# Optimization experiments

Hardware: AMD Instinct MI355X
Metric: run time of the kernel (lower is better)

Reference implementation:

```python
import jax, jax.numpy as jnp
import numpy as np

B, T, IMG = 64, 20, 64
IN_DIM = IMG * IMG          # 4096, from x.view(B,-1,64*64)
C_IN = 8                    # input_channels
R_DIM = C_IN * 1024         # 8192, reshape(B,20,-1,32,32) constraint
NF = 64                     # num_filters
Z_DIM = 256
LIN_IN = 2 * NF * 7 * 7     # 6272


def setup_inputs() -> dict:
    key = jax.random.key(0)
    ks = jax.random.split(key, 10)
    x = jax.random.normal(ks[0], (B, T, IMG, IMG), jnp.float32)
    Win = jax.random.normal(ks[1], (IN_DIM, R_DIM), jnp.float32) / np.sqrt(IN_DIM).astype(np.float32)
    U = jax.random.normal(ks[2], (IN_DIM, R_DIM), jnp.float32) / np.sqrt(IN_DIM).astype(np.float32)
    Wr = jax.random.normal(ks[3], (R_DIM, R_DIM), jnp.float32) / np.sqrt(R_DIM).astype(np.float32)
    conv1_w = jax.random.normal(ks[4], (NF, C_IN, 3, 3, 3), jnp.float32) * 0.05
    conv1_b = jax.random.normal(ks[5], (NF,), jnp.float32) * 0.01
    conv2_w = jax.random.normal(ks[6], (2 * NF, NF, 3, 4, 4), jnp.float32) * 0.05
    conv2_b = jax.random.normal(ks[7], (2 * NF,), jnp.float32) * 0.01
    lin_w = jax.random.normal(ks[8], (Z_DIM, LIN_IN), jnp.float32) * 0.02
    lin_b = jax.random.normal(ks[9], (Z_DIM,), jnp.float32) * 0.01
    return {"x": x, "Win": Win, "U": U, "Wr": Wr,
            "conv1_w": conv1_w, "conv1_b": conv1_b,
            "conv2_w": conv2_w, "conv2_b": conv2_b,
            "lin_w": lin_w, "lin_b": lin_b}


def reference(x, Win, U, Wr, conv1_w, conv1_b, conv2_w, conv2_b, lin_w, lin_b):
    Bn = x.shape[0]
    xf = x.reshape(Bn, T, IN_DIM)                      # (B,T,4096)
    h0 = jnp.tanh(xf[:, 0] @ Win)                      # (B,R)
    xU = jnp.einsum('bti,ir->tbr', xf[:, 1:], U)       # precompute input drive (T-1,B,R)

    def step(h, xu):
        h = jnp.tanh(xu + h @ Wr)
        return h, h

    _, hs = jax.lax.scan(step, h0, xU)                 # (T-1,B,R)
    H = jnp.concatenate([h0[None], hs], axis=0)        # (T,B,R)
    H = jnp.swapaxes(H, 0, 1)                          # (B,T,R)

    h = H.reshape(Bn, T, C_IN, 32, 32).transpose(0, 2, 1, 3, 4)  # (B,C,T,32,32)
    dn = ('NCDHW', 'OIDHW', 'NCDHW')
    y = jax.lax.conv_general_dilated(h, conv1_w, (1, 2, 2),
                                     [(1, 1), (1, 1), (1, 1)], dimension_numbers=dn)
    y = y + conv1_b[None, :, None, None, None]
    y = jax.nn.leaky_relu(y, 0.01)                     # (B,NF,20,16,16)
    y = jax.lax.conv_general_dilated(y, conv2_w, (1, 2, 2),
                                     [(1, 1), (0, 0), (0, 0)], dimension_numbers=dn)
    y = y + conv2_b[None, :, None, None, None]
    y = jax.nn.leaky_relu(y, 0.01)                     # (B,2NF,20,7,7)

    y = y.reshape(Bn, -1, T, LIN_IN)                   # (B,1,20,6272), same row-major view as torch
    y = y @ lin_w.T + lin_b                            # (B,1,20,Z_DIM)
    mu, log_var = jnp.split(y, 2, axis=3)
    return mu, log_var
```

## Files before the change

### kernel.cpp

```cpp
#include <hip/hip_runtime.h>

typedef __bf16 v8bf __attribute__((ext_vector_type(8)));
typedef float  v4f  __attribute__((ext_vector_type(4)));
typedef unsigned short us8 __attribute__((ext_vector_type(8)));

__device__ __forceinline__ float bf2f(unsigned short u) {
    union { unsigned int i; float f; } v; v.i = ((unsigned int)u) << 16; return v.f;
}
__device__ __forceinline__ unsigned short f2bf(float f) {
    union { float f; unsigned int i; } v; v.f = f;
    return (unsigned short)((v.i + 0x7fffu + ((v.i >> 16) & 1u)) >> 16);
}
__device__ __forceinline__ int sw(int b) { return b ^ (((b >> 7) & 7) << 4); }

__global__ __launch_bounds__(256)
void transpose_f32_bf16(const float* __restrict__ src,
                        unsigned short* __restrict__ dst, int K, int N)
{
    __shared__ unsigned short tile[64][72];
    const int tid = threadIdx.x;
    const int c0 = blockIdx.x * 64, r0 = blockIdx.y * 64;
    const int tr = tid >> 2, tc4 = tid & 3;
    const float* sp = src + (size_t)(r0 + tr) * N + c0 + tc4 * 16;
#pragma unroll
    for (int j = 0; j < 4; ++j) {
        v4f f = *reinterpret_cast<const v4f*>(sp + j * 4);
#pragma unroll
        for (int e = 0; e < 4; ++e) tile[tr][tc4 * 16 + j * 4 + e] = f2bf(f[e]);
    }
    __syncthreads();
    const int ow = tid >> 3, och = tid & 7;
#pragma unroll
    for (int p = 0; p < 2; ++p) {
        int orow = p * 32 + ow;
        us8 o;
#pragma unroll
        for (int e = 0; e < 8; ++e) o[e] = tile[och * 8 + e][orow];
        *reinterpret_cast<us8*>(dst + (size_t)(c0 + orow) * K + r0 + och * 8) = o;
    }
}

template<int BN, bool STORE_BF16, bool AF32, bool BF32>
__global__ __launch_bounds__(256, 2)
void gemm_bt(const void* __restrict__ Ap, int lda_lo, int lda_hi,
             const void* __restrict__ BTp, int ldb,
             void* __restrict__ Cout, int ldc,
             int ksub, long long csplit_stride)
{
    constexpr int FN  = BN / 32;
    constexpr int BCH = BN / 32;
    const int tid = threadIdx.x;
    const int lane = tid & 63, wid = tid >> 6;
    const int wr = wid >> 1, wc = wid & 1;
    const int nt = blockIdx.x, mt = blockIdx.y, kz = blockIdx.z;
    const int n0 = nt * BN;
    const int kstart = kz * ksub;

    __shared__ unsigned short smem[(64 + BN) * 64];
    char* As = reinterpret_cast<char*>(smem);
    char* Bs = reinterpret_cast<char*>(smem + 64 * 64);

    const unsigned short* A16 = (const unsigned short*)Ap;
    const float*          A32 = (const float*)Ap;
    const unsigned short* B16 = (const unsigned short*)BTp;
    const float*          B32 = (const float*)BTp;

    const int arow = AF32 ? (tid >> 2) : (tid >> 3);
    const int aq   = AF32 ? (tid & 3) : (tid & 7);
    const float* Ab32 = A32 + (size_t)arow * lda_lo + (size_t)mt * lda_hi + kstart + aq * 16;
    const unsigned short* Ab16 = A16 + (size_t)arow * lda_lo + (size_t)mt * lda_hi + kstart + aq * 8;
    const int brow = tid >> 3, bq = tid & 7;
    const float* Bb32 = B32 + (size_t)(n0 + brow) * ldb + kstart + bq * 8;
    const unsigned short* Bb16 = B16 + (size_t)(n0 + brow) * ldb + kstart + bq * 8;

    v4f fa[4];
    us8 ra[2];
    v4f fb[BCH][2];
    us8 rb[BCH];

    auto load = [&](int kk) {
        if (AF32) {
#pragma unroll
            for (int j = 0; j < 4; ++j)
                fa[j] = *reinterpret_cast<const v4f*>(Ab32 + kk + j * 4);
        } else {
#pragma unroll
            for (int p = 0; p < 2; ++p)
                ra[p] = *reinterpret_cast<const us8*>(Ab16 + (size_t)(p * 32) * lda_lo + kk);
        }
        if (BF32) {
#pragma unroll
            for (int p = 0; p < BCH; ++p) {
                fb[p][0] = *reinterpret_cast<const v4f*>(Bb32 + (size_t)(p * 32) * ldb + kk);
                fb[p][1] = *reinterpret_cast<const v4f*>(Bb32 + (size_t)(p * 32) * ldb + kk + 4);
            }
        } else {
#pragma unroll
            for (int p = 0; p < BCH; ++p)
                rb[p] = *reinterpret_cast<const us8*>(Bb16 + (size_t)(p * 32) * ldb + kk);
        }
    };
    auto stage = [&]() {
        if (AF32) {
#pragma unroll
            for (int h = 0; h < 2; ++h) {
                us8 v;
#pragma unroll
                for (int e = 0; e < 8; ++e) v[e] = f2bf(fa[h * 2 + (e >> 2)][e & 3]);
                *reinterpret_cast<us8*>(As + arow * 128 + (((aq * 2 + h) * 16) ^ ((arow & 7) << 4))) = v;
            }
        } else {
#pragma unroll
            for (int p = 0; p < 2; ++p)
                *reinterpret_cast<us8*>(As + (arow + p * 32) * 128 + ((aq * 16) ^ ((arow & 7) << 4))) = ra[p];
        }
#pragma unroll
        for (int p = 0; p < BCH; ++p) {
            us8 v;
            if (BF32) {
#pragma unroll
                for (int e = 0; e < 8; ++e) v[e] = f2bf(fb[p][e >> 2][e & 3]);
            } else v = rb[p];
            *reinterpret_cast<us8*>(Bs + (brow + p * 32) * 128 + ((bq * 16) ^ ((brow & 7) << 4))) = v;
        }
    };

    v4f z4 = {0.f, 0.f, 0.f, 0.f};
    v4f acc[2][FN];
#pragma unroll
    for (int i = 0; i < 2; ++i)
#pragma unroll
        for (int j = 0; j < FN; ++j) acc[i][j] = z4;

    const int l15 = lane & 15, l4 = lane >> 4;
    const int nk = ksub / 64;
    load(0);
    for (int it = 0; it < nk; ++it) {
        __syncthreads();
        stage();
        __syncthreads();
        if (it + 1 < nk) load((it + 1) * 64);
#pragma unroll
        for (int ks = 0; ks < 2; ++ks) {
            const int kb = (ks * 32 + l4 * 8) * 2;
            v8bf af[2], bfr[FN];
#pragma unroll
            for (int fm = 0; fm < 2; ++fm) {
                int row = wr * 32 + fm * 16 + l15;
                af[fm] = *reinterpret_cast<const v8bf*>(As + row * 128 + (kb ^ ((row & 7) << 4)));
            }
#pragma unroll
            for (int fn = 0; fn < FN; ++fn) {
                int row = wc * (BN / 2) + fn * 16 + l15;
                bfr[fn] = *reinterpret_cast<const v8bf*>(Bs + row * 128 + (kb ^ ((row & 7) << 4)));
            }
#pragma unroll
            for (int fm = 0; fm < 2; ++fm)
#pragma unroll
                for (int fn = 0; fn < FN; ++fn)
                    acc[fm][fn] = __builtin_amdgcn_mfma_f32_16x16x32_bf16(af[fm], bfr[fn], acc[fm][fn], 0, 0, 0);
        }
    }
    const long long m0 = (long long)mt * 64;
#pragma unroll
    for (int fm = 0; fm < 2; ++fm)
#pragma unroll
        for (int fn = 0; fn < FN; ++fn)
#pragma unroll
            for (int r = 0; r < 4; ++r) {
                long long row = m0 + wr * 32 + fm * 16 + l4 * 4 + r;
                long long col = n0 + wc * (BN / 2) + fn * 16 + l15;
                long long idx = (long long)kz * csplit_stride + row * ldc + col;
                if (STORE_BF16) reinterpret_cast<unsigned short*>(Cout)[idx] = f2bf(acc[fm][fn][r]);
                else            reinterpret_cast<float*>(Cout)[idx]          = acc[fm][fn][r];
            }
}

__global__ __launch_bounds__(256)
void scan_combine(const float* __restrict__ part, int nparts,
                  const unsigned short* __restrict__ xu,
                  unsigned short* __restrict__ hcur,
                  unsigned short* __restrict__ Hbf, int t)
{
    int i = blockIdx.x * 256 + threadIdx.x;
    float pre = xu ? bf2f(xu[i]) : 0.f;
    for (int z = 0; z < nparts; ++z) pre += part[(size_t)z * 524288 + i];
    float h = tanhf(pre);
    unsigned short hb = f2bf(h);
    hcur[i] = hb;
    int b = i >> 13, r = i & 8191;
    int c = r >> 10, pp = r & 1023;
    Hbf[(((size_t)b * 20 + t) * 1024 + pp) * 8 + c] = hb;
}

#define KZ 4
__global__ __launch_bounds__(256, 2)
void scan_step(const unsigned short* __restrict__ WrT,
               const unsigned short* __restrict__ hprev,
               const unsigned short* __restrict__ xu,
               unsigned short* __restrict__ hnext,
               unsigned short* __restrict__ Hbf, int t,
               float* __restrict__ part,
               unsigned int* __restrict__ tickets)
{
    const int tid = threadIdx.x, lane = tid & 63, wid = tid >> 6;
    const int wr = wid >> 1, wc = wid & 1;
    const int nt = blockIdx.x & 127, kz = blockIdx.x >> 7;
    const int n0 = nt * 64, kstart = kz * 2048;
    const int l15 = lane & 15, l4 = lane >> 4;

    __shared__ unsigned short smem[16384];
    char* base = reinterpret_cast<char*>(smem);

    const int srow = tid >> 3, sq = tid & 7;
    const int gslot = sq ^ (srow & 7);
    const unsigned short* Asrc = hprev + (size_t)srow * 8192 + kstart + gslot * 8;
    const unsigned short* Bsrc = WrT + (size_t)(n0 + srow) * 8192 + kstart + gslot * 8;

    auto stage = [&](int buf, int kk) {
        char* dA = base + buf * 16384 + wid * 1024;
        char* dB = dA + 8192;
#pragma unroll
        for (int p = 0; p < 2; ++p) {
            __builtin_amdgcn_global_load_lds(
                (const __attribute__((address_space(1))) void*)(Asrc + kk + (size_t)p * 32 * 8192),
                (__attribute__((address_space(3))) void*)(dA + p * 4096), 16, 0, 0);
            __builtin_amdgcn_global_load_lds(
                (const __attribute__((address_space(1))) void*)(Bsrc + kk + (size_t)p * 32 * 8192),
                (__attribute__((address_space(3))) void*)(dB + p * 4096), 16, 0, 0);
        }
    };

    v4f acc00 = {0.f, 0.f, 0.f, 0.f};
    v4f acc01 = acc00, acc10 = acc00, acc11 = acc00;

    stage(0, 0);
    for (int it = 0; it < 32; ++it) {
        const int cur = it & 1;
        __syncthreads();
        if (it + 1 < 32) stage(cur ^ 1, (it + 1) * 64);
        const char* As = base + cur * 16384;
        const char* Bs = As + 8192;
#pragma unroll
        for (int ks = 0; ks < 2; ++ks) {
            const int kb = (ks * 32 + l4 * 8) * 2;
            v8bf a0, a1, b0, b1;
            { int row = wr * 32 + l15;      a0 = *reinterpret_cast<const v8bf*>(As + row * 128 + (kb ^ ((row & 7) << 4))); }
            { int row = wr * 32 + 16 + l15; a1 = *reinterpret_cast<const v8bf*>(As + row * 128 + (kb ^ ((row & 7) << 4))); }
            { int row = wc * 32 + l15;      b0 = *reinterpret_cast<const v8bf*>(Bs + row * 128 + (kb ^ ((row & 7) << 4))); }
            { int row = wc * 32 + 16 + l15; b1 = *reinterpret_cast<const v8bf*>(Bs + row * 128 + (kb ^ ((row & 7) << 4))); }
            acc00 = __builtin_amdgcn_mfma_f32_16x16x32_bf16(a0, b0, acc00, 0, 0, 0);
            acc01 = __builtin_amdgcn_mfma_f32_16x16x32_bf16(a0, b1, acc01, 0, 0, 0);
            acc10 = __builtin_amdgcn_mfma_f32_16x16x32_bf16(a1, b0, acc10, 0, 0, 0);
            acc11 = __builtin_amdgcn_mfma_f32_16x16x32_bf16(a1, b1, acc11, 0, 0, 0);
        }
    }

    float* mypart = part + (size_t)kz * 524288;
#pragma unroll
    for (int r = 0; r < 4; ++r) {
        int row0 = wr * 32 + l4 * 4 + r;
        int col0 = n0 + wc * 32 + l15;
        mypart[(size_t)row0 * 8192 + col0]             = acc00[r];
        mypart[(size_t)row0 * 8192 + col0 + 16]        = acc01[r];
        mypart[(size_t)(row0 + 16) * 8192 + col0]      = acc10[r];
        mypart[(size_t)(row0 + 16) * 8192 + col0 + 16] = acc11[r];
    }

    __shared__ int lastflag;
    __syncthreads();
    if (tid == 0) {
        unsigned int old = __hip_atomic_fetch_add(&tickets[nt], 1u,
                              __ATOMIC_ACQ_REL, __HIP_MEMORY_SCOPE_AGENT);
        lastflag = (old == KZ - 1);
    }
    __syncthreads();
    if (!lastflag) return;

    const int row = tid >> 2;
    const int c0 = n0 + (tid & 3) * 16;
    float pre[16];
    {
        const us8* xp = reinterpret_cast<const us8*>(xu + (size_t)row * 8192 + c0);
        us8 x0 = xp[0], x1 = xp[1];
#pragma unroll
        for (int j = 0; j < 8; ++j) { pre[j] = bf2f(x0[j]); pre[8 + j] = bf2f(x1[j]); }
    }
#pragma unroll
    for (int z = 0; z < KZ; ++z) {
        const float* pp = part + (size_t)z * 524288 + (size_t)row * 8192 + c0;
#pragma unroll
        for (int q = 0; q < 4; ++q) {
            v4f v = *reinterpret_cast<const v4f*>(pp + q * 4);
#pragma unroll
            for (int e = 0; e < 4; ++e) pre[q * 4 + e] += v[e];
        }
    }
    us8 o0, o1;
#pragma unroll
    for (int j = 0; j < 16; ++j) {
        unsigned short hb = f2bf(tanhf(pre[j]));
        if (j < 8) o0[j] = hb; else o1[j - 8] = hb;
        int col = c0 + j;
        Hbf[(((size_t)row * 20 + t) * 1024 + (col & 1023)) * 8 + (col >> 10)] = hb;
    }
    *reinterpret_cast<us8*>(hnext + (size_t)row * 8192 + c0)     = o0;
    *reinterpret_cast<us8*>(hnext + (size_t)row * 8192 + c0 + 8) = o1;
    if (tid == 0)
        __hip_atomic_store(&tickets[nt], 0u, __ATOMIC_RELAXED, __HIP_MEMORY_SCOPE_AGENT);
}

__global__ __launch_bounds__(256)
void cvt_w1(const float* __restrict__ w, unsigned short* __restrict__ o,
            unsigned int* __restrict__ tickets)
{
    if (blockIdx.x == 0 && threadIdx.x < 128) tickets[threadIdx.x] = 0;
    int idx = blockIdx.x * 256 + threadIdx.x;
    if (idx >= 64 * 224) return;
    int co = idx / 224, k = idx % 224;
    int g = k >> 3, ci = k & 7;
    float v = 0.f;
    if (g < 27) {
        int dt = g / 9, rr = g % 9, dy = rr / 3, dx = rr % 3;
        v = w[(((co * 8 + ci) * 3 + dt) * 3 + dy) * 3 + dx];
    }
    o[idx] = f2bf(v);
}
__global__ __launch_bounds__(256)
void cvt_w2(const float* __restrict__ w, unsigned short* __restrict__ o)
{
    int idx = blockIdx.x * 256 + threadIdx.x;
    if (idx >= 128 * 3072) return;
    int co = idx / 3072, k = idx % 3072;
    int g = k >> 6, ci = k & 63;
    int dt = g >> 4, dy = (g >> 2) & 3, dx = g & 3;
    o[idx] = f2bf(w[(((co * 64 + ci) * 3 + dt) * 4 + dy) * 4 + dx]);
}

__global__ __launch_bounds__(256, 2)
void conv1_kernel(const unsigned short* __restrict__ H,
                  const unsigned short* __restrict__ w1,
                  const float* __restrict__ bias,
                  unsigned short* __restrict__ y1)
{
    const int b = blockIdx.x, t = blockIdx.y;
    const int tid = threadIdx.x, lane = tid & 63, wid = tid >> 6;
    __shared__ unsigned short in_s[3 * 33 * 33 * 8];
    __shared__ unsigned short w_s[64 * 224];

    for (int i = tid; i < 13068; i += 256) reinterpret_cast<unsigned int*>(in_s)[i] = 0;
    __syncthreads();
    for (int idx = tid; idx < 3 * 1024; idx += 256) {
        int dt = idx >> 10, rem = idx & 1023;
        int iy = rem >> 5, ix = rem & 31;
        int ts = t + dt - 1;
        if (ts >= 0 && ts < 20) {
            us8 v = *reinterpret_cast<const us8*>(H + (((size_t)b * 20 + ts) * 1024 + rem) * 8);
            int byte = ((dt * 33 + iy + 1) * 33 + (ix + 1)) * 16;
            *reinterpret_cast<us8*>(reinterpret_cast<char*>(in_s) + sw(byte)) = v;
        }
    }
    for (int idx = tid; idx < 64 * 28; idx += 256) {
        int co = idx / 28, j = idx % 28;
        us8 v = *reinterpret_cast<const us8*>(w1 + co * 224 + j * 8);
        *reinterpret_cast<us8*>(reinterpret_cast<char*>(w_s) + sw(co * 448 + j * 16)) = v;
    }
    __syncthreads();

    const int l15 = lane & 15, l4 = lane >> 4;
    const int m_lo = wid * 64 + l15;
    v4f z4 = {0.f, 0.f, 0.f, 0.f};
    v4f acc[4][4];
#pragma unroll
    for (int i = 0; i < 4; ++i)
#pragma unroll
        for (int j = 0; j < 4; ++j) acc[i][j] = z4;

#pragma unroll
    for (int ks = 0; ks < 7; ++ks) {
        int g = ks * 4 + l4;
        int gc = g < 27 ? g : 26;
        int dt = gc / 9, rr = gc % 9, dy = rr / 3, dx = rr % 3;
        v8bf ap[4], aw[4];
#pragma unroll
        for (int fm = 0; fm < 4; ++fm) {
            int m = fm * 16 + m_lo;
            int py = m >> 4, px = m & 15;
            int byte = ((dt * 33 + 2 * py + dy) * 33 + 2 * px + dx) * 16;
            ap[fm] = *reinterpret_cast<const v8bf*>(reinterpret_cast<const char*>(in_s) + sw(byte));
        }
        int kb2 = (ks * 32 + l4 * 8) * 2;
#pragma unroll
        for (int fc = 0; fc < 4; ++fc) {
            int co = fc * 16 + l15;
            aw[fc] = *reinterpret_cast<const v8bf*>(reinterpret_cast<const char*>(w_s) + sw(co * 448 + kb2));
        }
#pragma unroll
        for (int fm = 0; fm < 4; ++fm)
#pragma unroll
            for (int fc = 0; fc < 4; ++fc)
                acc[fm][fc] = __builtin_amdgcn_mfma_f32_16x16x32_bf16(ap[fm], aw[fc], acc[fm][fc], 0, 0, 0);
    }
#pragma unroll
    for (int fm = 0; fm < 4; ++fm)
#pragma unroll
        for (int fc = 0; fc < 4; ++fc)
#pragma unroll
            for (int r = 0; r < 4; ++r) {
                int m  = wid * 64 + fm * 16 + l4 * 4 + r;
                int co = fc * 16 + l15;
                float v = acc[fm][fc][r] + bias[co];
                v = v > 0.f ? v : 0.01f * v;
                y1[(((size_t)b * 20 + t) * 256 + m) * 64 + co] = f2bf(v);
            }
}

__global__ __launch_bounds__(512, 2)
void conv2_kernel(const unsigned short* __restrict__ y1,
                  const unsigned short* __restrict__ w2,
                  const float* __restrict__ bias,
                  unsigned short* __restrict__ y2)
{
    const int b = blockIdx.x, t = blockIdx.y;
    const int tid = threadIdx.x, lane = tid & 63, wid = tid >> 6;
    const int wc = wid >> 1, wr = wid & 1;
    __shared__ unsigned short in_s[256 * 64];
    __shared__ unsigned short w_s[128 * 128];
    const int l15 = lane & 15, l4 = lane >> 4;

    const int m0v = wr * 32 + l15, m1v = m0v + 16;
    const int m0c = m0v < 49 ? m0v : 48, m1c = m1v < 49 ? m1v : 48;
    const int py0 = m0c / 7, px0 = m0c - py0 * 7;
    const int py1 = m1c / 7, px1 = m1c - py1 * 7;

    v4f acc[2][2];
#pragma unroll
    for (int i = 0; i < 2; ++i)
#pragma unroll
        for (int j = 0; j < 2; ++j) acc[i][j] = (v4f){0.f, 0.f, 0.f, 0.f};

    for (int dt = 0; dt < 3; ++dt) {
        int ts = t + dt - 1;
        __syncthreads();
        if (ts < 0 || ts >= 20) continue;
#pragma unroll
        for (int p = 0; p < 4; ++p) {
            int idx = tid + p * 512;
            int slot = idx >> 3, c8 = idx & 7;
            int yy = slot >> 4, xx = slot & 15;
            us8 v = *reinterpret_cast<const us8*>(y1 + (((size_t)b * 20 + ts) * 256 + slot) * 64 + c8 * 8);
            int cell = ((yy & 1) * 2 + (xx & 1)) * 64 + (yy >> 1) * 8 + (xx >> 1);
            int byte = cell * 128 + ((c8 * 16) ^ (((cell ^ (cell >> 3)) & 7) << 4));
            *reinterpret_cast<us8*>(reinterpret_cast<char*>(in_s) + byte) = v;
        }
        for (int kc = 0; kc < 8; ++kc) {
            __syncthreads();
#pragma unroll
            for (int p = 0; p < 4; ++p) {
                int idx = tid + p * 512;
                int co = idx >> 4, j = idx & 15;
                us8 v = *reinterpret_cast<const us8*>(w2 + (size_t)co * 3072 + dt * 1024 + kc * 128 + j * 8);
                *reinterpret_cast<us8*>(reinterpret_cast<char*>(w_s) + co * 256 + ((j * 16) ^ ((co & 7) << 4))) = v;
            }
            __syncthreads();
#pragma unroll
            for (int ks = 0; ks < 4; ++ks) {
                int klocal = ks * 32 + l4 * 8;
                int kk = kc * 128 + klocal;
                int dy = (kk >> 8) & 3, dx = (kk >> 6) & 3, ci0 = kk & 63;
                v8bf aw[2], bp[2];
#pragma unroll
                for (int fc = 0; fc < 2; ++fc) {
                    int co = wc * 32 + fc * 16 + l15;
                    aw[fc] = *reinterpret_cast<const v8bf*>(reinterpret_cast<const char*>(w_s)
                               + co * 256 + ((klocal * 2) ^ ((co & 7) << 4)));
                }
                int plane = ((dy & 1) << 1) | (dx & 1);
                int c0 = plane * 64 + (py0 + (dy >> 1)) * 8 + px0 + (dx >> 1);
                int c1 = plane * 64 + (py1 + (dy >> 1)) * 8 + px1 + (dx >> 1);
                bp[0] = *reinterpret_cast<const v8bf*>(reinterpret_cast<const char*>(in_s)
                          + c0 * 128 + ((ci0 * 2) ^ (((c0 ^ (c0 >> 3)) & 7) << 4)));
                bp[1] = *reinterpret_cast<const v8bf*>(reinterpret_cast<const char*>(in_s)
                          + c1 * 128 + ((ci0 * 2) ^ (((c1 ^ (c1 >> 3)) & 7) << 4)));
#pragma unroll
                for (int fc = 0; fc < 2; ++fc)
#pragma unroll
                    for (int fm = 0; fm < 2; ++fm)
                        acc[fc][fm] = __builtin_amdgcn_mfma_f32_16x16x32_bf16(aw[fc], bp[fm], acc[fc][fm], 0, 0, 0);
            }
        }
    }
#pragma unroll
    for (int fc = 0; fc < 2; ++fc)
#pragma unroll
        for (int fm = 0; fm < 2; ++fm)
#pragma unroll
            for (int r = 0; r < 4; ++r) {
                int co = wc * 32 + fc * 16 + l4 * 4 + r;
                int m  = wr * 32 + fm * 16 + l15;
                if (m < 49) {
                    float v = acc[fc][fm][r] + bias[co];
                    v = v > 0.f ? v : 0.01f * v;
                    y2[(((size_t)b * 128 + co) * 20 + t) * 49 + m] = f2bf(v);
                }
            }
}

__global__ __launch_bounds__(256)
void lin_epi(const float* __restrict__ linC, const float* __restrict__ lb,
             float* __restrict__ out)
{
    int i = blockIdx.x * 256 + threadIdx.x;
    int m = i >> 8, n = i & 255;
    float v = lb[n];
#pragma unroll
    for (int z = 0; z < 7; ++z) v += linC[(size_t)z * 327680 + i];
    size_t o = (n < 128) ? ((size_t)m * 128 + n) : (163840 + (size_t)m * 128 + (n - 128));
    out[o] = v;
}

extern "C" void kernel_launch(void* const* d_in, const int* in_sizes, int n_in,
                              void* d_out, int out_size, void* d_ws, size_t ws_size,
                              hipStream_t stream)
{
    const float* x   = (const float*)d_in[0];
    const float* Win = (const float*)d_in[1];
    const float* U   = (const float*)d_in[2];
    const float* Wr  = (const float*)d_in[3];
    const float* c1w = (const float*)d_in[4];
    const float* c1b = (const float*)d_in[5];
    const float* c2w = (const float*)d_in[6];
    const float* c2b = (const float*)d_in[7];
    const float* lw  = (const float*)d_in[8];
    const float* lb  = (const float*)d_in[9];

    char* ws = (char*)d_ws;
    unsigned short* WrT  = (unsigned short*)(ws);
    unsigned short* WT   = (unsigned short*)(ws + 134217728ll);
    unsigned short* y1   = (unsigned short*)(ws + 134217728ll);
    unsigned short* y2   = (unsigned short*)(ws + 176160768ll);
    unsigned short* XALL = (unsigned short*)(ws + 201326592ll);
    unsigned short* Hbf  = (unsigned short*)(ws + 222298112ll);
    unsigned short* hb0  = (unsigned short*)(ws + 243269632ll);
    unsigned short* hb1  = (unsigned short*)(ws + 244318208ll);
    float*          part = (float*)        (ws + 245366784ll);
    float*          linC = (float*)        (ws + 245366784ll);
    unsigned short* w1bf = (unsigned short*)(ws + 254541824ll);
    unsigned short* w2bf = (unsigned short*)(ws + 254570496ll);
    unsigned int*   tick = (unsigned int*) (ws + 255356928ll);
    float*          out  = (float*)d_out;

    cvt_w1<<<56, 256, 0, stream>>>(c1w, w1bf, tick);
    cvt_w2<<<1536, 256, 0, stream>>>(c2w, w2bf);

    transpose_f32_bf16<<<dim3(128, 64), 256, 0, stream>>>(Win, WT, 4096, 8192);
    gemm_bt<64, false, true, false><<<dim3(128, 1, 4), 256, 0, stream>>>(
        x, 81920, 0, WT, 4096, part, 8192, 1024, 524288ll);
    scan_combine<<<2048, 256, 0, stream>>>(part, 4, (const unsigned short*)nullptr, hb0, Hbf, 0);

    transpose_f32_bf16<<<dim3(128, 64), 256, 0, stream>>>(U, WT, 4096, 8192);
    gemm_bt<128, true, true, false><<<dim3(64, 19, 1), 256, 0, stream>>>(
        x + 4096, 81920, 4096, WT, 4096, XALL + 524288, 8192, 4096, 0ll);

    transpose_f32_bf16<<<dim3(128, 128), 256, 0, stream>>>(Wr, WrT, 8192, 8192);
    for (int t = 1; t < 20; ++t) {
        const unsigned short* hprev = (t & 1) ? hb0 : hb1;
        unsigned short*       hnext = (t & 1) ? hb1 : hb0;
        scan_step<<<512, 256, 0, stream>>>(WrT, hprev, XALL + (size_t)t * 524288,
                                           hnext, Hbf, t, part, tick);
    }

    conv1_kernel<<<dim3(64, 20), 256, 0, stream>>>(Hbf, w1bf, c1b, y1);
    conv2_kernel<<<dim3(64, 20), 512, 0, stream>>>(y1, w2bf, c2b, y2);

    gemm_bt<128, false, false, true><<<dim3(2, 20, 7), 256, 0, stream>>>(
        y2, 6272, 6272 * 64, lw, 6272, linC, 256, 896, 327680ll);
    lin_epi<<<1280, 256, 0, stream>>>(linC, lb, out);
}
```

Baseline: 1.455 ms.

## Deepen scan_step prefetch to 4 stages and reuse it for the h0 GEMM

```diff
diff --git a/kernel.cpp b/kernel.cpp
--- a/kernel.cpp
+++ b/kernel.cpp
@@ -38,6 +38,19 @@
         for (int e = 0; e < 8; ++e) o[e] = tile[och * 8 + e][orow];
         *reinterpret_cast<us8*>(dst + (size_t)(c0 + orow) * K + r0 + och * 8) = o;
     }
+}
+
+__global__ __launch_bounds__(256)
+void cvt_x(const float* __restrict__ x, unsigned short* __restrict__ xb)
+{
+    int i = blockIdx.x * 256 + threadIdx.x;
+    if (i >= 655360) return;
+    v4f f0 = *reinterpret_cast<const v4f*>(x + (size_t)i * 8);
+    v4f f1 = *reinterpret_cast<const v4f*>(x + (size_t)i * 8 + 4);
+    us8 o;
+#pragma unroll
+    for (int e = 0; e < 4; ++e) { o[e] = f2bf(f0[e]); o[4 + e] = f2bf(f1[e]); }
+    *reinterpret_cast<us8*>(xb + (size_t)i * 8) = o;
 }
 
 template<int BN, bool STORE_BF16, bool AF32, bool BF32>
@@ -176,27 +189,11 @@
             }
 }
 
-__global__ __launch_bounds__(256)
-void scan_combine(const float* __restrict__ part, int nparts,
-                  const unsigned short* __restrict__ xu,
-                  unsigned short* __restrict__ hcur,
-                  unsigned short* __restrict__ Hbf, int t)
-{
-    int i = blockIdx.x * 256 + threadIdx.x;
-    float pre = xu ? bf2f(xu[i]) : 0.f;
-    for (int z = 0; z < nparts; ++z) pre += part[(size_t)z * 524288 + i];
-    float h = tanhf(pre);
-    unsigned short hb = f2bf(h);
-    hcur[i] = hb;
-    int b = i >> 13, r = i & 8191;
-    int c = r >> 10, pp = r & 1023;
-    Hbf[(((size_t)b * 20 + t) * 1024 + pp) * 8 + c] = hb;
-}
-
 #define KZ 4
 __global__ __launch_bounds__(256, 2)
-void scan_step(const unsigned short* __restrict__ WrT,
-               const unsigned short* __restrict__ hprev,
+void scan_step(const unsigned short* __restrict__ A, int lda,
+               const unsigned short* __restrict__ BT, int ldb,
+               int kper,
                const unsigned short* __restrict__ xu,
                unsigned short* __restrict__ hnext,
                unsigned short* __restrict__ Hbf, int t,
@@ -206,16 +203,17 @@
     const int tid = threadIdx.x, lane = tid & 63, wid = tid >> 6;
     const int wr = wid >> 1, wc = wid & 1;
     const int nt = blockIdx.x & 127, kz = blockIdx.x >> 7;
-    const int n0 = nt * 64, kstart = kz * 2048;
+    const int n0 = nt * 64, kstart = kz * kper;
     const int l15 = lane & 15, l4 = lane >> 4;
-
-    __shared__ unsigned short smem[16384];
+    const int nit = kper >> 6;
+
+    __shared__ unsigned short smem[32768];
     char* base = reinterpret_cast<char*>(smem);
 
     const int srow = tid >> 3, sq = tid & 7;
     const int gslot = sq ^ (srow & 7);
-    const unsigned short* Asrc = hprev + (size_t)srow * 8192 + kstart + gslot * 8;
-    const unsigned short* Bsrc = WrT + (size_t)(n0 + srow) * 8192 + kstart + gslot * 8;
+    const unsigned short* Asrc = A + (size_t)srow * lda + kstart + gslot * 8;
+    const unsigned short* Bsrc = BT + (size_t)(n0 + srow) * ldb + kstart + gslot * 8;
 
     auto stage = [&](int buf, int kk) {
         char* dA = base + buf * 16384 + wid * 1024;
@@ -223,10 +221,10 @@
 #pragma unroll
         for (int p = 0; p < 2; ++p) {
             __builtin_amdgcn_global_load_lds(
-                (const __attribute__((address_space(1))) void*)(Asrc + kk + (size_t)p * 32 * 8192),
+                (const __attribute__((address_space(1))) void*)(Asrc + kk + (size_t)p * 32 * lda),
                 (__attribute__((address_space(3))) void*)(dA + p * 4096), 16, 0, 0);
             __builtin_amdgcn_global_load_lds(
-                (const __attribute__((address_space(1))) void*)(Bsrc + kk + (size_t)p * 32 * 8192),
+                (const __attribute__((address_space(1))) void*)(Bsrc + kk + (size_t)p * 32 * ldb),
                 (__attribute__((address_space(3))) void*)(dB + p * 4096), 16, 0, 0);
         }
     };
@@ -234,12 +232,16 @@
     v4f acc00 = {0.f, 0.f, 0.f, 0.f};
     v4f acc01 = acc00, acc10 = acc00, acc11 = acc00;
 
-    stage(0, 0);
-    for (int it = 0; it < 32; ++it) {
-        const int cur = it & 1;
-        __syncthreads();
-        if (it + 1 < 32) stage(cur ^ 1, (it + 1) * 64);
-        const char* As = base + cur * 16384;
+    stage(0, 0); stage(1, 64); stage(2, 128);
+    for (int it = 0; it < nit; ++it) {
+        const int ahead = nit - 1 - it;
+        if (ahead >= 2)      asm volatile("s_waitcnt vmcnt(8)" ::: "memory");
+        else if (ahead == 1) asm volatile("s_waitcnt vmcnt(4)" ::: "memory");
+        else                 asm volatile("s_waitcnt vmcnt(0)" ::: "memory");
+        __builtin_amdgcn_s_barrier();
+        __builtin_amdgcn_sched_barrier(0);
+        if (it + 3 < nit) stage((it + 3) & 3, (it + 3) * 64);
+        const char* As = base + (it & 3) * 16384;
         const char* Bs = As + 8192;
 #pragma unroll
         for (int ks = 0; ks < 2; ++ks) {
@@ -280,11 +282,14 @@
     const int row = tid >> 2;
     const int c0 = n0 + (tid & 3) * 16;
     float pre[16];
-    {
+    if (xu) {
         const us8* xp = reinterpret_cast<const us8*>(xu + (size_t)row * 8192 + c0);
         us8 x0 = xp[0], x1 = xp[1];
 #pragma unroll
         for (int j = 0; j < 8; ++j) { pre[j] = bf2f(x0[j]); pre[8 + j] = bf2f(x1[j]); }
+    } else {
+#pragma unroll
+        for (int j = 0; j < 16; ++j) pre[j] = 0.f;
     }
 #pragma unroll
     for (int z = 0; z < KZ; ++z) {
@@ -536,6 +541,7 @@
 
     char* ws = (char*)d_ws;
     unsigned short* WrT  = (unsigned short*)(ws);
+    unsigned short* xbf  = (unsigned short*)(ws);
     unsigned short* WT   = (unsigned short*)(ws + 134217728ll);
     unsigned short* y1   = (unsigned short*)(ws + 134217728ll);
     unsigned short* y2   = (unsigned short*)(ws + 176160768ll);
@@ -552,11 +558,11 @@
 
     cvt_w1<<<56, 256, 0, stream>>>(c1w, w1bf, tick);
     cvt_w2<<<1536, 256, 0, stream>>>(c2w, w2bf);
+    cvt_x<<<2560, 256, 0, stream>>>(x, xbf);
 
     transpose_f32_bf16<<<dim3(128, 64), 256, 0, stream>>>(Win, WT, 4096, 8192);
-    gemm_bt<64, false, true, false><<<dim3(128, 1, 4), 256, 0, stream>>>(
-        x, 81920, 0, WT, 4096, part, 8192, 1024, 524288ll);
-    scan_combine<<<2048, 256, 0, stream>>>(part, 4, (const unsigned short*)nullptr, hb0, Hbf, 0);
+    scan_step<<<512, 256, 0, stream>>>(xbf, 81920, WT, 4096, 1024,
+                                       (const unsigned short*)nullptr, hb0, Hbf, 0, part, tick);
 
     transpose_f32_bf16<<<dim3(128, 64), 256, 0, stream>>>(U, WT, 4096, 8192);
     gemm_bt<128, true, true, false><<<dim3(64, 19, 1), 256, 0, stream>>>(
@@ -566,8 +572,8 @@
     for (int t = 1; t < 20; ++t) {
         const unsigned short* hprev = (t & 1) ? hb0 : hb1;
         unsigned short*       hnext = (t & 1) ? hb1 : hb0;
-        scan_step<<<512, 256, 0, stream>>>(WrT, hprev, XALL + (size_t)t * 524288,
-                                           hnext, Hbf, t, part, tick);
+        scan_step<<<512, 256, 0, stream>>>(hprev, 8192, WrT, 8192, 2048,
+                                           XALL + (size_t)t * 524288, hnext, Hbf, t, part, tick);
     }
 
     conv1_kernel<<<dim3(64, 20), 256, 0, stream>>>(Hbf, w1bf, c1b, y1);
```

New measurement: 1.487 ms. 2.2% more time.

## Retile recurrent scan step to 64x128 tiles with 8-way split-K

Applied to the files above, without the earlier changes.

```diff
diff --git a/kernel.cpp b/kernel.cpp
--- a/kernel.cpp
+++ b/kernel.cpp
@@ -193,23 +193,23 @@
     Hbf[(((size_t)b * 20 + t) * 1024 + pp) * 8 + c] = hb;
 }
 
-#define KZ 4
-__global__ __launch_bounds__(256, 2)
-void scan_step(const unsigned short* __restrict__ WrT,
-               const unsigned short* __restrict__ hprev,
-               const unsigned short* __restrict__ xu,
-               unsigned short* __restrict__ hnext,
-               unsigned short* __restrict__ Hbf, int t,
-               float* __restrict__ part,
-               unsigned int* __restrict__ tickets)
+#define KZ8 8
+__global__ __launch_bounds__(256, 3)
+void scan_step3(const unsigned short* __restrict__ WrT,
+                const unsigned short* __restrict__ hprev,
+                const unsigned short* __restrict__ xu,
+                unsigned short* __restrict__ hnext,
+                unsigned short* __restrict__ Hbf, int t,
+                float* __restrict__ part,
+                unsigned int* __restrict__ tickets)
 {
     const int tid = threadIdx.x, lane = tid & 63, wid = tid >> 6;
     const int wr = wid >> 1, wc = wid & 1;
-    const int nt = blockIdx.x & 127, kz = blockIdx.x >> 7;
-    const int n0 = nt * 64, kstart = kz * 2048;
+    const int nt = blockIdx.x & 63, kz = blockIdx.x >> 6;
+    const int n0 = nt * 128, kstart = kz * 1024;
     const int l15 = lane & 15, l4 = lane >> 4;
 
-    __shared__ unsigned short smem[16384];
+    __shared__ unsigned short smem[24576];
     char* base = reinterpret_cast<char*>(smem);
 
     const int srow = tid >> 3, sq = tid & 7;
@@ -218,94 +218,110 @@
     const unsigned short* Bsrc = WrT + (size_t)(n0 + srow) * 8192 + kstart + gslot * 8;
 
     auto stage = [&](int buf, int kk) {
-        char* dA = base + buf * 16384 + wid * 1024;
-        char* dB = dA + 8192;
-#pragma unroll
-        for (int p = 0; p < 2; ++p) {
+        char* dA = base + buf * 24576 + wid * 1024;
+        char* dB = base + buf * 24576 + 8192 + wid * 1024;
+#pragma unroll
+        for (int p = 0; p < 2; ++p)
             __builtin_amdgcn_global_load_lds(
                 (const __attribute__((address_space(1))) void*)(Asrc + kk + (size_t)p * 32 * 8192),
                 (__attribute__((address_space(3))) void*)(dA + p * 4096), 16, 0, 0);
+#pragma unroll
+        for (int p = 0; p < 4; ++p)
             __builtin_amdgcn_global_load_lds(
                 (const __attribute__((address_space(1))) void*)(Bsrc + kk + (size_t)p * 32 * 8192),
                 (__attribute__((address_space(3))) void*)(dB + p * 4096), 16, 0, 0);
-        }
     };
 
-    v4f acc00 = {0.f, 0.f, 0.f, 0.f};
-    v4f acc01 = acc00, acc10 = acc00, acc11 = acc00;
+    v4f acc[2][4];
+#pragma unroll
+    for (int i = 0; i < 2; ++i)
+#pragma unroll
+        for (int j = 0; j < 4; ++j) acc[i][j] = (v4f){0.f, 0.f, 0.f, 0.f};
 
     stage(0, 0);
-    for (int it = 0; it < 32; ++it) {
+    for (int it = 0; it < 16; ++it) {
         const int cur = it & 1;
         __syncthreads();
-        if (it + 1 < 32) stage(cur ^ 1, (it + 1) * 64);
-        const char* As = base + cur * 16384;
+        if (it + 1 < 16) stage(cur ^ 1, (it + 1) * 64);
+        const char* As = base + cur * 24576;
         const char* Bs = As + 8192;
 #pragma unroll
         for (int ks = 0; ks < 2; ++ks) {
             const int kb = (ks * 32 + l4 * 8) * 2;
-            v8bf a0, a1, b0, b1;
-            { int row = wr * 32 + l15;      a0 = *reinterpret_cast<const v8bf*>(As + row * 128 + (kb ^ ((row & 7) << 4))); }
-            { int row = wr * 32 + 16 + l15; a1 = *reinterpret_cast<const v8bf*>(As + row * 128 + (kb ^ ((row & 7) << 4))); }
-            { int row = wc * 32 + l15;      b0 = *reinterpret_cast<const v8bf*>(Bs + row * 128 + (kb ^ ((row & 7) << 4))); }
-            { int row = wc * 32 + 16 + l15; b1 = *reinterpret_cast<const v8bf*>(Bs + row * 128 + (kb ^ ((row & 7) << 4))); }
-            acc00 = __builtin_amdgcn_mfma_f32_16x16x32_bf16(a0, b0, acc00, 0, 0, 0);
-            acc01 = __builtin_amdgcn_mfma_f32_16x16x32_bf16(a0, b1, acc01, 0, 0, 0);
-            acc10 = __builtin_amdgcn_mfma_f32_16x16x32_bf16(a1, b0, acc10, 0, 0, 0);
-            acc11 = __builtin_amdgcn_mfma_f32_16x16x32_bf16(a1, b1, acc11, 0, 0, 0);
+            v8bf af[2], bf[4];
+#pragma unroll
+            for (int fm = 0; fm < 2; ++fm) {
+                int row = wr * 32 + fm * 16 + l15;
+                af[fm] = *reinterpret_cast<const v8bf*>(As + row * 128 + (kb ^ ((row & 7) << 4)));
+            }
+#pragma unroll
+            for (int fn = 0; fn < 4; ++fn) {
+                int row = wc * 64 + fn * 16 + l15;
+                bf[fn] = *reinterpret_cast<const v8bf*>(Bs + row * 128 + (kb ^ ((row & 7) << 4)));
+            }
+#pragma unroll
+            for (int fm = 0; fm < 2; ++fm)
+#pragma unroll
+                for (int fn = 0; fn < 4; ++fn)
+                    acc[fm][fn] = __builtin_amdgcn_mfma_f32_16x16x32_bf16(af[fm], bf[fn], acc[fm][fn], 0, 0, 0);
         }
     }
 
     float* mypart = part + (size_t)kz * 524288;
 #pragma unroll
-    for (int r = 0; r < 4; ++r) {
-        int row0 = wr * 32 + l4 * 4 + r;
-        int col0 = n0 + wc * 32 + l15;
-        mypart[(size_t)row0 * 8192 + col0]             = acc00[r];
-        mypart[(size_t)row0 * 8192 + col0 + 16]        = acc01[r];
-        mypart[(size_t)(row0 + 16) * 8192 + col0]      = acc10[r];
-        mypart[(size_t)(row0 + 16) * 8192 + col0 + 16] = acc11[r];
-    }
+    for (int fm = 0; fm < 2; ++fm)
+#pragma unroll
+        for (int fn = 0; fn < 4; ++fn)
+#pragma unroll
+            for (int r = 0; r < 4; ++r) {
+                int row = wr * 32 + fm * 16 + l4 * 4 + r;
+                int col = n0 + wc * 64 + fn * 16 + l15;
+                mypart[(size_t)row * 8192 + col] = acc[fm][fn][r];
+            }
 
     __shared__ int lastflag;
     __syncthreads();
     if (tid == 0) {
         unsigned int old = __hip_atomic_fetch_add(&tickets[nt], 1u,
                               __ATOMIC_ACQ_REL, __HIP_MEMORY_SCOPE_AGENT);
-        lastflag = (old == KZ - 1);
+        lastflag = (old == KZ8 - 1);
     }
     __syncthreads();
     if (!lastflag) return;
 
     const int row = tid >> 2;
-    const int c0 = n0 + (tid & 3) * 16;
-    float pre[16];
+    const int c0 = n0 + (tid & 3) * 32;
+    float pre[32];
     {
         const us8* xp = reinterpret_cast<const us8*>(xu + (size_t)row * 8192 + c0);
-        us8 x0 = xp[0], x1 = xp[1];
-#pragma unroll
-        for (int j = 0; j < 8; ++j) { pre[j] = bf2f(x0[j]); pre[8 + j] = bf2f(x1[j]); }
-    }
-#pragma unroll
-    for (int z = 0; z < KZ; ++z) {
+#pragma unroll
+        for (int q = 0; q < 4; ++q) {
+            us8 xv = xp[q];
+#pragma unroll
+            for (int j = 0; j < 8; ++j) pre[q * 8 + j] = bf2f(xv[j]);
+        }
+    }
+#pragma unroll
+    for (int z = 0; z < KZ8; ++z) {
         const float* pp = part + (size_t)z * 524288 + (size_t)row * 8192 + c0;
 #pragma unroll
-        for (int q = 0; q < 4; ++q) {
+        for (int q = 0; q < 8; ++q) {
             v4f v = *reinterpret_cast<const v4f*>(pp + q * 4);
 #pragma unroll
             for (int e = 0; e < 4; ++e) pre[q * 4 + e] += v[e];
         }
     }
-    us8 o0, o1;
-#pragma unroll
-    for (int j = 0; j < 16; ++j) {
+    us8 o[4];
+#pragma unroll
+    for (int j = 0; j < 32; ++j) {
         unsigned short hb = f2bf(tanhf(pre[j]));
-        if (j < 8) o0[j] = hb; else o1[j - 8] = hb;
+        o[j >> 3][j & 7] = hb;
         int col = c0 + j;
         Hbf[(((size_t)row * 20 + t) * 1024 + (col & 1023)) * 8 + (col >> 10)] = hb;
     }
-    *reinterpret_cast<us8*>(hnext + (size_t)row * 8192 + c0)     = o0;
-    *reinterpret_cast<us8*>(hnext + (size_t)row * 8192 + c0 + 8) = o1;
+#pragma unroll
+    for (int q = 0; q < 4; ++q)
+        *reinterpret_cast<us8*>(hnext + (size_t)row * 8192 + c0 + q * 8) = o[q];
     if (tid == 0)
         __hip_atomic_store(&tickets[nt], 0u, __ATOMIC_RELAXED, __HIP_MEMORY_SCOPE_AGENT);
 }
@@ -538,6 +554,7 @@
     unsigned short* WrT  = (unsigned short*)(ws);
     unsigned short* WT   = (unsigned short*)(ws + 134217728ll);
     unsigned short* y1   = (unsigned short*)(ws + 134217728ll);
+    float*          part16 = (float*)      (ws + 176160768ll);
     unsigned short* y2   = (unsigned short*)(ws + 176160768ll);
     unsigned short* XALL = (unsigned short*)(ws + 201326592ll);
     unsigned short* Hbf  = (unsigned short*)(ws + 222298112ll);
@@ -566,8 +583,8 @@
     for (int t = 1; t < 20; ++t) {
         const unsigned short* hprev = (t & 1) ? hb0 : hb1;
         unsigned short*       hnext = (t & 1) ? hb1 : hb0;
-        scan_step<<<512, 256, 0, stream>>>(WrT, hprev, XALL + (size_t)t * 524288,
-                                           hnext, Hbf, t, part, tick);
+        scan_step3<<<512, 256, 0, stream>>>(WrT, hprev, XALL + (size_t)t * 524288,
+                                            hnext, Hbf, t, part16, tick);
     }
 
     conv1_kernel<<<dim3(64, 20), 256, 0, stream>>>(Hbf, w1bf, c1b, y1);
```

Measured after the change: 2.113 ms. 45.2% more time.
